# Kernel optimization log

Hardware: AMD Instinct MI355X
Metric: run time of the kernel (lower is better)

Reference implementation:

```python
import jax, jax.numpy as jnp
import numpy as np

N = 100000          # nodes
E = 1600000         # edges
F = 128             # input features
H = 128             # hidden_channels
G = 64              # graphs in batch


def setup_inputs() -> dict:
    key = jax.random.key(0)
    ks = jax.random.split(key, 16)
    x = jax.random.normal(ks[0], (N, F), dtype=jnp.float32)
    edge_index = jax.random.randint(ks[1], (2, E), 0, N, dtype=jnp.int32)
    batch = jnp.sort(jax.random.randint(ks[2], (N,), 0, G, dtype=jnp.int32))

    def glorot(k, fan_in, fan_out):
        s = jnp.sqrt(6.0 / (fan_in + fan_out)).astype(jnp.float32)
        return jax.random.uniform(k, (fan_in, fan_out), jnp.float32, -s, s)

    return {
        "x": x, "edge_index": edge_index, "batch": batch,
        "W1": glorot(ks[3], F, H),       "b1": jnp.zeros((H,), jnp.float32),
        "W2": glorot(ks[4], H, H),       "b2": jnp.zeros((H,), jnp.float32),
        "W3": glorot(ks[5], H, 2 * H),   "b3": jnp.zeros((2 * H,), jnp.float32),
        "W4": glorot(ks[6], 2 * H, H),   "b4": jnp.zeros((H,), jnp.float32),
        "Wl": glorot(ks[7], F, H),       "bl": jnp.zeros((H,), jnp.float32),
    }


def _gcn_conv(x, W, b, src, dst, deg_inv_sqrt):
    # PyG GCNConv: add self-loops, symmetric normalization D^-1/2 (A+I) D^-1/2
    h = x @ W                                  # [N, out]
    norm = deg_inv_sqrt[src] * deg_inv_sqrt[dst]      # [E]
    msg = h[src] * norm[:, None]               # gather + scale, [E, out]
    agg = jax.ops.segment_sum(msg, dst, num_segments=N)
    agg = agg + h * (deg_inv_sqrt * deg_inv_sqrt)[:, None]  # self-loop term (norm = 1/deg)
    return agg + b


def reference(x, edge_index, batch, W1, b1, W2, b2, W3, b3, W4, b4, Wl, bl):
    src, dst = edge_index[0], edge_index[1]
    # degree (incl. self-loop) from dst, as in PyG gcn_norm
    deg = jax.ops.segment_sum(jnp.ones((E,), jnp.float32), dst, num_segments=N) + 1.0
    deg_inv_sqrt = jax.lax.rsqrt(deg)

    identity = x
    x = jax.nn.relu(_gcn_conv(x, W1, b1, src, dst, deg_inv_sqrt))
    x = jax.nn.relu(_gcn_conv(x, W2, b2, src, dst, deg_inv_sqrt))
    x = jax.nn.relu(_gcn_conv(x, W3, b3, src, dst, deg_inv_sqrt))
    x = _gcn_conv(x, W4, b4, src, dst, deg_inv_sqrt)
    x = x + (identity @ Wl + bl)

    # global_mean_pool over graph ids
    sums = jax.ops.segment_sum(x, batch, num_segments=G)
    cnts = jax.ops.segment_sum(jnp.ones((N,), jnp.float32), batch, num_segments=G)
    return sums / jnp.maximum(cnts, 1.0)[:, None]
```

## Files before the change

### kernel.cpp

```cpp
#include <hip/hip_runtime.h>

#define NN 100000
#define EE 1600000
#define GG 64

typedef __attribute__((ext_vector_type(8))) short short8v;
typedef __attribute__((ext_vector_type(4))) float f32x4;

__device__ __forceinline__ unsigned short f2bf(float f) {
    unsigned u = __float_as_uint(f);
    u = (u + 0x7FFFu + ((u >> 16) & 1)) >> 16;
    return (unsigned short)u;
}
__device__ __forceinline__ float bf2f(unsigned short s) {
    return __uint_as_float((unsigned)s << 16);
}

__global__ __launch_bounds__(256) void count_kernel(const int* __restrict__ dst,
                                                    int* __restrict__ cnt) {
    int e = blockIdx.x * 256 + threadIdx.x;
    if (e < EE) atomicAdd(&cnt[dst[e]], 1);
}

__global__ __launch_bounds__(256) void dis_kernel(const int* __restrict__ cnt,
                                                  float* __restrict__ dis) {
    int i = blockIdx.x * 256 + threadIdx.x;
    if (i < NN) dis[i] = rsqrtf((float)cnt[i] + 1.0f);
}

#define SCAN_EPB 1024
__global__ __launch_bounds__(256) void scan_block_kernel(const int* __restrict__ in,
                                                         int* __restrict__ out,
                                                         int* __restrict__ bsums) {
    __shared__ int sd[256];
    int t = threadIdx.x;
    int base = blockIdx.x * SCAN_EPB + t * 4;
    int v[4];
#pragma unroll
    for (int j = 0; j < 4; ++j) v[j] = (base + j < NN) ? in[base + j] : 0;
    int s = v[0] + v[1] + v[2] + v[3];
    sd[t] = s;
    __syncthreads();
    for (int off = 1; off < 256; off <<= 1) {
        int add = (t >= off) ? sd[t - off] : 0;
        __syncthreads();
        sd[t] += add;
        __syncthreads();
    }
    int ex = sd[t] - s;
    int run = ex;
#pragma unroll
    for (int j = 0; j < 4; ++j) {
        if (base + j < NN) out[base + j] = run;
        run += v[j];
    }
    if (t == 255) bsums[blockIdx.x] = sd[255];
}

__global__ void scan_sums_kernel(int* __restrict__ bsums, int nb) {
    if (threadIdx.x == 0 && blockIdx.x == 0) {
        int run = 0;
        for (int i = 0; i < nb; ++i) {
            int v = bsums[i];
            bsums[i] = run;
            run += v;
        }
    }
}

__global__ __launch_bounds__(256) void scan_add_kernel(int* __restrict__ rs,
                                                       const int* __restrict__ bsums,
                                                       int* __restrict__ cursor) {
    int i = blockIdx.x * 256 + threadIdx.x;
    if (i < NN) {
        int v = rs[i] + bsums[i >> 10];
        rs[i] = v;
        cursor[i] = v;
    }
    if (i == 0) rs[NN] = EE;
}

__global__ __launch_bounds__(256) void scatter_kernel(const int* __restrict__ src,
                                                      const int* __restrict__ dst,
                                                      int* __restrict__ cursor,
                                                      int* __restrict__ csr) {
    int e = blockIdx.x * 256 + threadIdx.x;
    if (e < EE) {
        int d = dst[e];
        int p = atomicAdd(&cursor[d], 1);
        csr[p] = src[e];
    }
}

__global__ __launch_bounds__(256) void cvt_kernel(const float* __restrict__ x,
                                                  const float* __restrict__ dis,
                                                  unsigned short* __restrict__ xb) {
    size_t i = ((size_t)blockIdx.x * 256 + threadIdx.x) * 8;
    float d = dis[i >> 7];
    float4 a = *(const float4*)(x + i);
    float4 b = *(const float4*)(x + i + 4);
    short8v v;
    v[0] = (short)f2bf(a.x * d); v[1] = (short)f2bf(a.y * d);
    v[2] = (short)f2bf(a.z * d); v[3] = (short)f2bf(a.w * d);
    v[4] = (short)f2bf(b.x * d); v[5] = (short)f2bf(b.y * d);
    v[6] = (short)f2bf(b.z * d); v[7] = (short)f2bf(b.w * d);
    *(short8v*)(xb + i) = v;
}

template <int K, int M>
__global__ __launch_bounds__(64) void packw_kernel(const float* __restrict__ W,
                                                   unsigned short* __restrict__ Wp) {
    const int NKS = K / 32;
    int ct = blockIdx.x / NKS, ks = blockIdx.x % NKS;
    int lane = threadIdx.x;
    int col = ct * 16 + (lane & 15);
    int kb = ks * 32 + (lane >> 4) * 8;
    unsigned short* o = Wp + ((size_t)(ct * NKS + ks) * 64 + lane) * 16;
#pragma unroll
    for (int i = 0; i < 8; ++i) {
        float f = W[(size_t)(kb + i) * M + col];
        unsigned short h = f2bf(f);
        unsigned short l = f2bf(f - bf2f(h));
        o[i] = h;
        o[8 + i] = l;
    }
}

template <int K, int M, int RT, bool ASPLIT, bool RELU, bool BIAS, bool ACCUM, bool DSCALE>
__global__ __launch_bounds__(256) void gemm_kernel(const void* __restrict__ Ain,
                                                   const unsigned short* __restrict__ Wp,
                                                   const float* __restrict__ bias,
                                                   const float* __restrict__ dis,
                                                   void* __restrict__ out) {
    const int NKS = K / 32;
    int tid = threadIdx.x;
    int wave = tid >> 6, lane = tid & 63;
    int r0 = blockIdx.x * (RT * 64) + wave * (RT * 16);

    short8v ah[RT][NKS];
    short8v al[ASPLIT ? RT : 1][ASPLIT ? NKS : 1];
#pragma unroll
    for (int t = 0; t < RT; ++t) {
        int ra = r0 + t * 16 + (lane & 15);
        if (ra > NN - 1) ra = NN - 1;
        if (ASPLIT) {
            const float* A = (const float*)Ain;
#pragma unroll
            for (int ks = 0; ks < NKS; ++ks) {
                const float* p = A + (size_t)ra * K + ks * 32 + (lane >> 4) * 8;
                float4 v0 = *(const float4*)p;
                float4 v1 = *(const float4*)(p + 4);
                float f[8] = {v0.x, v0.y, v0.z, v0.w, v1.x, v1.y, v1.z, v1.w};
#pragma unroll
                for (int i = 0; i < 8; ++i) {
                    unsigned short h = f2bf(f[i]);
                    ah[t][ks][i] = (short)h;
                    al[t][ks][i] = (short)f2bf(f[i] - bf2f(h));
                }
            }
        } else {
            const unsigned short* A = (const unsigned short*)Ain;
#pragma unroll
            for (int ks = 0; ks < NKS; ++ks)
                ah[t][ks] = *(const short8v*)(A + (size_t)ra * K + ks * 32 + (lane >> 4) * 8);
        }
    }

    float dsc[RT][4];
#pragma unroll
    for (int t = 0; t < RT; ++t)
#pragma unroll
        for (int i = 0; i < 4; ++i) {
            int row = r0 + t * 16 + (lane >> 4) * 4 + i;
            dsc[t][i] = (DSCALE && row < NN) ? dis[row] : 1.f;
        }

#pragma unroll
    for (int ct = 0; ct < 8; ++ct) {
        int ctg = blockIdx.y * 8 + ct;
        int col = ctg * 16 + (lane & 15);
        float bv = BIAS ? bias[col] : 0.f;
        f32x4 acc[RT];
#pragma unroll
        for (int t = 0; t < RT; ++t) {
            acc[t][0] = bv; acc[t][1] = bv; acc[t][2] = bv; acc[t][3] = bv;
        }
#pragma unroll
        for (int ks = 0; ks < NKS; ++ks) {
            const short8v* pW = (const short8v*)Wp + ((size_t)(ctg * NKS + ks) * 64 + lane) * 2;
            short8v bh = pW[0], blo = pW[1];
#pragma unroll
            for (int t = 0; t < RT; ++t) {
                acc[t] = __builtin_amdgcn_mfma_f32_16x16x32_bf16(ah[t][ks], bh, acc[t], 0, 0, 0);
                acc[t] = __builtin_amdgcn_mfma_f32_16x16x32_bf16(ah[t][ks], blo, acc[t], 0, 0, 0);
                if (ASPLIT)
                    acc[t] = __builtin_amdgcn_mfma_f32_16x16x32_bf16(al[t][ks], bh, acc[t], 0, 0, 0);
            }
        }
#pragma unroll
        for (int t = 0; t < RT; ++t)
#pragma unroll
            for (int i = 0; i < 4; ++i) {
                int row = r0 + t * 16 + (lane >> 4) * 4 + i;
                if (row >= NN) continue;
                float v = acc[t][i];
                if (RELU) v = fmaxf(v, 0.f);
                if (ACCUM) {
                    ((float*)out)[(size_t)row * M + col] += v;
                } else {
                    ((unsigned short*)out)[(size_t)row * M + col] = f2bf(v * dsc[t][i]);
                }
            }
    }
}

template <int OUTMODE>
__global__ __launch_bounds__(256) void aggb_kernel(const unsigned short* __restrict__ h,
                                                   const float* __restrict__ dis,
                                                   const int* __restrict__ csr,
                                                   const int* __restrict__ rs,
                                                   const float* __restrict__ bias,
                                                   void* __restrict__ out) {
    int node = blockIdx.x * 4 + (threadIdx.x >> 6);
    int lane = threadIdx.x & 63;
    if (node >= NN) return;
    int c = lane & 15;
    int s = lane >> 4;
    int beg = rs[node], end = rs[node + 1];
    const uint4* hb = (const uint4*)h;
    float acc[8] = {};
    for (int e0 = beg; e0 < end; e0 += 16) {
        float m[4];
        uint4 v[4];
#pragma unroll
        for (int j = 0; j < 4; ++j) {
            int ej = e0 + j * 4 + s;
            int ec = ej < end ? ej : end - 1;
            int sidx = csr[ec];
            m[j] = ej < end ? 1.f : 0.f;
            v[j] = hb[(size_t)sidx * 16 + c];
        }
#pragma unroll
        for (int j = 0; j < 4; ++j) {
            acc[0] = fmaf(m[j], __uint_as_float(v[j].x << 16), acc[0]);
            acc[1] = fmaf(m[j], __uint_as_float(v[j].x & 0xFFFF0000u), acc[1]);
            acc[2] = fmaf(m[j], __uint_as_float(v[j].y << 16), acc[2]);
            acc[3] = fmaf(m[j], __uint_as_float(v[j].y & 0xFFFF0000u), acc[3]);
            acc[4] = fmaf(m[j], __uint_as_float(v[j].z << 16), acc[4]);
            acc[5] = fmaf(m[j], __uint_as_float(v[j].z & 0xFFFF0000u), acc[5]);
            acc[6] = fmaf(m[j], __uint_as_float(v[j].w << 16), acc[6]);
            acc[7] = fmaf(m[j], __uint_as_float(v[j].w & 0xFFFF0000u), acc[7]);
        }
    }
#pragma unroll
    for (int i = 0; i < 8; ++i) {
        acc[i] += __shfl_xor(acc[i], 16, 64);
        acc[i] += __shfl_xor(acc[i], 32, 64);
    }
    if (s == 0) {
        float d = dis[node];
        uint4 us = hb[(size_t)node * 16 + c];
        float sf[8];
        sf[0] = __uint_as_float(us.x << 16); sf[1] = __uint_as_float(us.x & 0xFFFF0000u);
        sf[2] = __uint_as_float(us.y << 16); sf[3] = __uint_as_float(us.y & 0xFFFF0000u);
        sf[4] = __uint_as_float(us.z << 16); sf[5] = __uint_as_float(us.z & 0xFFFF0000u);
        sf[6] = __uint_as_float(us.w << 16); sf[7] = __uint_as_float(us.w & 0xFFFF0000u);
        float r[8];
#pragma unroll
        for (int i = 0; i < 8; ++i) r[i] = d * (acc[i] + sf[i]);
        if (OUTMODE == 0) {
            uint4 o;
            o.x = (unsigned)f2bf(r[0]) | ((unsigned)f2bf(r[1]) << 16);
            o.y = (unsigned)f2bf(r[2]) | ((unsigned)f2bf(r[3]) << 16);
            o.z = (unsigned)f2bf(r[4]) | ((unsigned)f2bf(r[5]) << 16);
            o.w = (unsigned)f2bf(r[6]) | ((unsigned)f2bf(r[7]) << 16);
            ((uint4*)out)[(size_t)node * 16 + c] = o;
        } else {
#pragma unroll
            for (int i = 0; i < 8; ++i) r[i] += bias[c * 8 + i];
            float4 o0 = make_float4(r[0], r[1], r[2], r[3]);
            float4 o1 = make_float4(r[4], r[5], r[6], r[7]);
            float* O = (float*)out + (size_t)node * 128 + c * 8;
            *(float4*)O = o0;
            *(float4*)(O + 4) = o1;
        }
    }
}

__global__ __launch_bounds__(128) void pool_partial_kernel(const float* __restrict__ y,
                                                           const int* __restrict__ batch,
                                                           float* __restrict__ P) {
    int c = threadIdx.x;
    int chunk = (NN + gridDim.x - 1) / gridDim.x;
    int n0 = blockIdx.x * chunk;
    int n1 = n0 + chunk;
    if (n1 > NN) n1 = NN;
    if (n0 >= NN) return;
    int curg = batch[n0];
    float acc = 0.f;
    for (int n = n0; n < n1; ++n) {
        int g = batch[n];
        if (g != curg) {
            atomicAdd(&P[curg * 128 + c], acc);
            acc = 0.f;
            curg = g;
        }
        acc += y[(size_t)n * 128 + c];
    }
    atomicAdd(&P[curg * 128 + c], acc);
}

__global__ __launch_bounds__(128) void pool_final_kernel(const float* __restrict__ P,
                                                         const int* __restrict__ batch,
                                                         float* __restrict__ out) {
    int g = blockIdx.x, c = threadIdx.x;
    int lo = 0, hi = NN;
    while (lo < hi) {
        int m = (lo + hi) >> 1;
        if (batch[m] < g) lo = m + 1;
        else hi = m;
    }
    int start = lo;
    int lo2 = start, hi2 = NN;
    while (lo2 < hi2) {
        int m = (lo2 + hi2) >> 1;
        if (batch[m] < g + 1) lo2 = m + 1;
        else hi2 = m;
    }
    float cntg = (float)(lo2 - start);
    out[g * 128 + c] = P[g * 128 + c] / fmaxf(cntg, 1.f);
}

extern "C" void kernel_launch(void* const* d_in, const int* in_sizes, int n_in,
                              void* d_out, int out_size, void* d_ws, size_t ws_size,
                              hipStream_t stream) {
    const float* x = (const float*)d_in[0];
    const int* ei = (const int*)d_in[1];
    const int* batch = (const int*)d_in[2];
    const float* W1 = (const float*)d_in[3];
    const float* b1 = (const float*)d_in[4];
    const float* W2 = (const float*)d_in[5];
    const float* b2 = (const float*)d_in[6];
    const float* W3 = (const float*)d_in[7];
    const float* b3 = (const float*)d_in[8];
    const float* W4 = (const float*)d_in[9];
    const float* b4 = (const float*)d_in[10];
    const float* Wl = (const float*)d_in[11];
    const float* bl = (const float*)d_in[12];
    float* out = (float*)d_out;

    char* p = (char*)d_ws;
    auto alloc = [&](size_t bytes) {
        void* r = (void*)p;
        p += (bytes + 255) & ~(size_t)255;
        return r;
    };
    int* cnt = (int*)alloc((size_t)NN * 4);
    int* rs = (int*)alloc((size_t)(NN + 1) * 4);
    int* cursor = (int*)alloc((size_t)NN * 4);
    float* dis = (float*)alloc((size_t)NN * 4);
    const int NB = (NN + SCAN_EPB - 1) / SCAN_EPB;
    int* bsums = (int*)alloc((size_t)NB * 4);
    int* csr = (int*)alloc((size_t)EE * 4);
    unsigned short* xb = (unsigned short*)alloc((size_t)NN * 128 * 2);
    unsigned short* AG = (unsigned short*)alloc((size_t)NN * 128 * 2);
    unsigned short* GM = (unsigned short*)alloc((size_t)NN * 128 * 2);
    unsigned short* H3 = (unsigned short*)alloc((size_t)NN * 256 * 2);
    float* Y = (float*)alloc((size_t)NN * 128 * 4);
    unsigned short* W1p = (unsigned short*)alloc(8 * 4 * 64 * 16 * 2);
    unsigned short* W2p = (unsigned short*)alloc(8 * 4 * 64 * 16 * 2);
    unsigned short* W3p = (unsigned short*)alloc(16 * 4 * 64 * 16 * 2);
    unsigned short* W4p = (unsigned short*)alloc(8 * 8 * 64 * 16 * 2);
    unsigned short* Wlp = (unsigned short*)alloc(8 * 4 * 64 * 16 * 2);
    float* P = (float*)alloc((size_t)GG * 128 * 4);

    const int* src = ei;
    const int* dst = ei + EE;

    hipMemsetAsync(cnt, 0, (size_t)NN * 4, stream);
    hipMemsetAsync(P, 0, (size_t)GG * 128 * 4, stream);

    count_kernel<<<EE / 256, 256, 0, stream>>>(dst, cnt);
    dis_kernel<<<(NN + 255) / 256, 256, 0, stream>>>(cnt, dis);
    cvt_kernel<<<(NN * 128) / (256 * 8), 256, 0, stream>>>(x, dis, xb);
    scan_block_kernel<<<NB, 256, 0, stream>>>(cnt, rs, bsums);
    scan_sums_kernel<<<1, 64, 0, stream>>>(bsums, NB);
    scan_add_kernel<<<(NN + 255) / 256, 256, 0, stream>>>(rs, bsums, cursor);
    scatter_kernel<<<EE / 256, 256, 0, stream>>>(src, dst, cursor, csr);

    packw_kernel<128, 128><<<8 * 4, 64, 0, stream>>>(W1, W1p);
    packw_kernel<128, 128><<<8 * 4, 64, 0, stream>>>(W2, W2p);
    packw_kernel<128, 256><<<16 * 4, 64, 0, stream>>>(W3, W3p);
    packw_kernel<256, 128><<<8 * 8, 64, 0, stream>>>(W4, W4p);
    packw_kernel<128, 128><<<8 * 4, 64, 0, stream>>>(Wl, Wlp);

    const int AGG_GRID = (NN + 3) / 4;
    const int GX4 = (NN + 255) / 256;
    const int GX2 = (NN + 127) / 128;

    aggb_kernel<0><<<AGG_GRID, 256, 0, stream>>>(xb, dis, csr, rs, nullptr, AG);
    gemm_kernel<128, 128, 4, false, true, true, false, true><<<dim3(GX4, 1), 256, 0, stream>>>(AG, W1p, b1, dis, GM);
    aggb_kernel<0><<<AGG_GRID, 256, 0, stream>>>(GM, dis, csr, rs, nullptr, AG);
    gemm_kernel<128, 128, 4, false, true, true, false, true><<<dim3(GX4, 1), 256, 0, stream>>>(AG, W2p, b2, dis, GM);
    aggb_kernel<0><<<AGG_GRID, 256, 0, stream>>>(GM, dis, csr, rs, nullptr, AG);
    gemm_kernel<128, 256, 4, false, true, true, false, false><<<dim3(GX4, 2), 256, 0, stream>>>(AG, W3p, b3, nullptr, H3);
    gemm_kernel<256, 128, 2, false, false, false, false, true><<<dim3(GX2, 1), 256, 0, stream>>>(H3, W4p, nullptr, dis, AG);
    aggb_kernel<1><<<AGG_GRID, 256, 0, stream>>>(AG, dis, csr, rs, b4, Y);
    gemm_kernel<128, 128, 2, true, false, true, true, false><<<dim3(GX2, 1), 256, 0, stream>>>(x, Wlp, bl, nullptr, Y);
    pool_partial_kernel<<<512, 128, 0, stream>>>(Y, batch, P);
    pool_final_kernel<<<GG, 128, 0, stream>>>(P, batch, out);
}
```

Measured before the change: 824.8 us.

## Bucket-partition edges before CSR scatter and widen aggregation gather to 32 edges

Replaces the per-edge count and global-atomic scatter with a two-pass partition: each block bins its edge chunk by destination bucket into a staging buffer, then one block per bucket scatters those edges into CSR for better atomic and write locality. The aggregation kernel now gathers 8 neighbor rows per lane per iteration with predicated loads and plain adds instead of masked FMAs, increasing memory-level parallelism. The bucket scatter uses only 196 blocks with serial per-thread loops, which may limit parallelism, and it reuses the Y buffer as staging.

```diff
diff --git a/kernel.cpp b/kernel.cpp
--- a/kernel.cpp
+++ b/kernel.cpp
@@ -3,6 +3,9 @@
 #define NN 100000
 #define EE 1600000
 #define GG 64
+#define PBLK 391
+#define PCHUNK 4096
+#define NBUCK 196
 
 typedef __attribute__((ext_vector_type(8))) short short8v;
 typedef __attribute__((ext_vector_type(4))) float f32x4;
@@ -16,10 +19,43 @@
     return __uint_as_float((unsigned)s << 16);
 }
 
-__global__ __launch_bounds__(256) void count_kernel(const int* __restrict__ dst,
-                                                    int* __restrict__ cnt) {
-    int e = blockIdx.x * 256 + threadIdx.x;
-    if (e < EE) atomicAdd(&cnt[dst[e]], 1);
+__global__ __launch_bounds__(256) void partitionA_kernel(const int* __restrict__ src,
+                                                         const int* __restrict__ dst,
+                                                         int* __restrict__ cnt,
+                                                         int* __restrict__ ghist,
+                                                         int* __restrict__ gboff,
+                                                         int2* __restrict__ stage) {
+    __shared__ int hist[NBUCK];
+    __shared__ int boff[NBUCK];
+    __shared__ int bcur[NBUCK];
+    int b = blockIdx.x, t = threadIdx.x;
+    int e0 = b * PCHUNK;
+    int n = EE - e0;
+    if (n > PCHUNK) n = PCHUNK;
+    for (int i = t; i < NBUCK; i += 256) { hist[i] = 0; bcur[i] = 0; }
+    __syncthreads();
+    for (int i = t; i < n; i += 256) {
+        int d = dst[e0 + i];
+        atomicAdd(&cnt[d], 1);
+        atomicAdd(&hist[d >> 9], 1);
+    }
+    __syncthreads();
+    if (t == 0) {
+        int run = 0;
+        for (int k = 0; k < NBUCK; ++k) { boff[k] = run; run += hist[k]; }
+    }
+    __syncthreads();
+    for (int i = t; i < n; i += 256) {
+        int d = dst[e0 + i];
+        int sv = src[e0 + i];
+        int k = d >> 9;
+        int p = boff[k] + atomicAdd(&bcur[k], 1);
+        stage[(size_t)b * PCHUNK + p] = make_int2(sv, d);
+    }
+    for (int k = t; k < NBUCK; k += 256) {
+        ghist[b * NBUCK + k] = hist[k];
+        gboff[b * NBUCK + k] = boff[k];
+    }
 }
 
 __global__ __launch_bounds__(256) void dis_kernel(const int* __restrict__ cnt,
@@ -80,15 +116,20 @@
     if (i == 0) rs[NN] = EE;
 }
 
-__global__ __launch_bounds__(256) void scatter_kernel(const int* __restrict__ src,
-                                                      const int* __restrict__ dst,
-                                                      int* __restrict__ cursor,
-                                                      int* __restrict__ csr) {
-    int e = blockIdx.x * 256 + threadIdx.x;
-    if (e < EE) {
-        int d = dst[e];
-        int p = atomicAdd(&cursor[d], 1);
-        csr[p] = src[e];
+__global__ __launch_bounds__(256) void scatterC_kernel(const int2* __restrict__ stage,
+                                                       const int* __restrict__ ghist,
+                                                       const int* __restrict__ gboff,
+                                                       int* __restrict__ cursor,
+                                                       int* __restrict__ csr) {
+    int k = blockIdx.x;
+    for (int b = threadIdx.x; b < PBLK; b += 256) {
+        int c_ = ghist[b * NBUCK + k];
+        size_t base = (size_t)b * PCHUNK + gboff[b * NBUCK + k];
+        for (int i = 0; i < c_; ++i) {
+            int2 e = stage[base + i];
+            int p = atomicAdd(&cursor[e.y], 1);
+            csr[p] = e.x;
+        }
     }
 }
 
@@ -229,27 +270,24 @@
     int beg = rs[node], end = rs[node + 1];
     const uint4* hb = (const uint4*)h;
     float acc[8] = {};
-    for (int e0 = beg; e0 < end; e0 += 16) {
-        float m[4];
-        uint4 v[4];
-#pragma unroll
-        for (int j = 0; j < 4; ++j) {
+    for (int e0 = beg; e0 < end; e0 += 32) {
+        uint4 v[8];
+#pragma unroll
+        for (int j = 0; j < 8; ++j) {
+            v[j] = make_uint4(0u, 0u, 0u, 0u);
             int ej = e0 + j * 4 + s;
-            int ec = ej < end ? ej : end - 1;
-            int sidx = csr[ec];
-            m[j] = ej < end ? 1.f : 0.f;
-            v[j] = hb[(size_t)sidx * 16 + c];
-        }
-#pragma unroll
-        for (int j = 0; j < 4; ++j) {
-            acc[0] = fmaf(m[j], __uint_as_float(v[j].x << 16), acc[0]);
-            acc[1] = fmaf(m[j], __uint_as_float(v[j].x & 0xFFFF0000u), acc[1]);
-            acc[2] = fmaf(m[j], __uint_as_float(v[j].y << 16), acc[2]);
-            acc[3] = fmaf(m[j], __uint_as_float(v[j].y & 0xFFFF0000u), acc[3]);
-            acc[4] = fmaf(m[j], __uint_as_float(v[j].z << 16), acc[4]);
-            acc[5] = fmaf(m[j], __uint_as_float(v[j].z & 0xFFFF0000u), acc[5]);
-            acc[6] = fmaf(m[j], __uint_as_float(v[j].w << 16), acc[6]);
-            acc[7] = fmaf(m[j], __uint_as_float(v[j].w & 0xFFFF0000u), acc[7]);
+            if (ej < end) v[j] = hb[(size_t)csr[ej] * 16 + c];
+        }
+#pragma unroll
+        for (int j = 0; j < 8; ++j) {
+            acc[0] += __uint_as_float(v[j].x << 16);
+            acc[1] += __uint_as_float(v[j].x & 0xFFFF0000u);
+            acc[2] += __uint_as_float(v[j].y << 16);
+            acc[3] += __uint_as_float(v[j].y & 0xFFFF0000u);
+            acc[4] += __uint_as_float(v[j].z << 16);
+            acc[5] += __uint_as_float(v[j].z & 0xFFFF0000u);
+            acc[6] += __uint_as_float(v[j].w << 16);
+            acc[7] += __uint_as_float(v[j].w & 0xFFFF0000u);
         }
     }
 #pragma unroll
@@ -362,6 +400,8 @@
     const int NB = (NN + SCAN_EPB - 1) / SCAN_EPB;
     int* bsums = (int*)alloc((size_t)NB * 4);
     int* csr = (int*)alloc((size_t)EE * 4);
+    int* ghist = (int*)alloc((size_t)PBLK * NBUCK * 4);
+    int* gboff = (int*)alloc((size_t)PBLK * NBUCK * 4);
     unsigned short* xb = (unsigned short*)alloc((size_t)NN * 128 * 2);
     unsigned short* AG = (unsigned short*)alloc((size_t)NN * 128 * 2);
     unsigned short* GM = (unsigned short*)alloc((size_t)NN * 128 * 2);
@@ -373,6 +413,7 @@
     unsigned short* W4p = (unsigned short*)alloc(8 * 8 * 64 * 16 * 2);
     unsigned short* Wlp = (unsigned short*)alloc(8 * 4 * 64 * 16 * 2);
     float* P = (float*)alloc((size_t)GG * 128 * 4);
+    int2* stage = (int2*)Y;
 
     const int* src = ei;
     const int* dst = ei + EE;
@@ -380,13 +421,13 @@
     hipMemsetAsync(cnt, 0, (size_t)NN * 4, stream);
     hipMemsetAsync(P, 0, (size_t)GG * 128 * 4, stream);
 
-    count_kernel<<<EE / 256, 256, 0, stream>>>(dst, cnt);
+    partitionA_kernel<<<PBLK, 256, 0, stream>>>(src, dst, cnt, ghist, gboff, stage);
     dis_kernel<<<(NN + 255) / 256, 256, 0, stream>>>(cnt, dis);
     cvt_kernel<<<(NN * 128) / (256 * 8), 256, 0, stream>>>(x, dis, xb);
     scan_block_kernel<<<NB, 256, 0, stream>>>(cnt, rs, bsums);
     scan_sums_kernel<<<1, 64, 0, stream>>>(bsums, NB);
     scan_add_kernel<<<(NN + 255) / 256, 256, 0, stream>>>(rs, bsums, cursor);
-    scatter_kernel<<<EE / 256, 256, 0, stream>>>(src, dst, cursor, csr);
+    scatterC_kernel<<<NBUCK, 256, 0, stream>>>(stage, ghist, gboff, cursor, csr);
 
     packw_kernel<128, 128><<<8 * 4, 64, 0, stream>>>(W1, W1p);
     packw_kernel<128, 128><<<8 * 4, 64, 0, stream>>>(W2, W2p);
```

After: 844.2 us. 1.02x slower.
